# Kernel tuning notes

Hardware: AMD Instinct MI355X
Metric: run time of the kernel (lower is better)

Reference implementation:

```python
import jax, jax.numpy as jnp
import numpy as np

HIDDEN = 2048  # hidden_size; also key seq length (required by span_param broadcast)
BATCH = 4
SEQ = 2048


def setup_inputs() -> dict:
    key = jax.random.key(0)
    kq, kk, kv = jax.random.split(key, 3)
    return {
        "query": jax.random.normal(kq, (BATCH, SEQ, HIDDEN), dtype=jnp.float32),
        "key": jax.random.normal(kk, (BATCH, SEQ, HIDDEN), dtype=jnp.float32),
        "value": jax.random.normal(kv, (BATCH, SEQ, HIDDEN), dtype=jnp.float32),
        "span_param": jnp.ones((1, HIDDEN), dtype=jnp.float32),  # nn.Parameter init torch.ones
    }


def reference(query, key, value, span_param):
    # scores: [B, Sq, Sk]
    scale = 1.0 / jnp.sqrt(jnp.asarray(query.shape[-1], query.dtype))
    scores = jnp.einsum("bqd,bkd->bqk", query, key) * scale
    # elementwise learned gate broadcast over last axis (Sk == hidden_size)
    scores = scores * jax.nn.sigmoid(span_param)
    weights = jax.nn.softmax(scores, axis=-1)
    return jnp.einsum("bqk,bkd->bqd", weights, value)
```

## Files before the change

kernel.cpp:

```cpp
#include <hip/hip_runtime.h>
#include <math.h>


#define SEQ 2048
#define HID 2048
#define NB 4

typedef __attribute__((ext_vector_type(8))) __bf16 bf16x8;
typedef __attribute__((ext_vector_type(4))) float f32x4;
typedef __attribute__((ext_vector_type(8))) unsigned short ushort8;

#define GLD16(src, dst)                                              \
  __builtin_amdgcn_global_load_lds(                                  \
      (const __attribute__((address_space(1))) void*)(src),          \
      (__attribute__((address_space(3))) void*)(dst), 16, 0, 0)

__device__ __forceinline__ unsigned short f2bf(float f) {
  unsigned u = __float_as_uint(f);
  u += 0x7fffu + ((u >> 16) & 1u);
  return (unsigned short)(u >> 16);
}

__global__ __launch_bounds__(256) void cvt_kernel(
    const float* __restrict__ in, unsigned short* __restrict__ out, int n) {
  size_t stride = (size_t)gridDim.x * blockDim.x * 8;
  for (size_t i = ((size_t)blockIdx.x * blockDim.x + threadIdx.x) * 8;
       i < (size_t)n; i += stride) {
    float4 v0 = *reinterpret_cast<const float4*>(in + i);
    float4 v1 = *reinterpret_cast<const float4*>(in + i + 4);
    ushort8 o;
    o[0] = f2bf(v0.x); o[1] = f2bf(v0.y); o[2] = f2bf(v0.z); o[3] = f2bf(v0.w);
    o[4] = f2bf(v1.x); o[5] = f2bf(v1.y); o[6] = f2bf(v1.z); o[7] = f2bf(v1.w);
    *reinterpret_cast<ushort8*>(out + i) = o;
  }
}

__global__ __launch_bounds__(256) void tcvt_kernel(
    const float* __restrict__ V, unsigned short* __restrict__ Vt) {
  __shared__ unsigned short tile[64][65];
  int b = blockIdx.z;
  int k0 = blockIdx.x * 64;
  int d0 = blockIdx.y * 64;
  const float* src = V + ((size_t)b * SEQ + k0) * HID + d0;
  unsigned short* dst = Vt + ((size_t)b * HID + d0) * SEQ + k0;
  int t = threadIdx.x;
#pragma unroll
  for (int i = 0; i < 4; ++i) {
    int j = i * 256 + t;
    int r = j >> 4;
    int c = (j & 15) * 4;
    float4 v = *reinterpret_cast<const float4*>(src + (size_t)r * HID + c);
    tile[c + 0][r] = f2bf(v.x);
    tile[c + 1][r] = f2bf(v.y);
    tile[c + 2][r] = f2bf(v.z);
    tile[c + 3][r] = f2bf(v.w);
  }
  __syncthreads();
#pragma unroll
  for (int i = 0; i < 2; ++i) {
    int j = i * 256 + t;
    int r = j >> 3;
    int c = (j & 7) * 8;
    ushort8 o;
#pragma unroll
    for (int e = 0; e < 8; ++e) o[e] = tile[r][c + e];
    *reinterpret_cast<ushort8*>(dst + (size_t)r * SEQ + c) = o;
  }
}

__global__ __launch_bounds__(256) void gemm1_kernel(
    const unsigned short* __restrict__ Q, const unsigned short* __restrict__ K,
    unsigned short* __restrict__ E, float* __restrict__ Z,
    const float* __restrict__ span) {
  __shared__ __align__(16) unsigned short Asm[128 * 64];
  __shared__ __align__(16) unsigned short Bsm[128 * 64];
  int bid = blockIdx.x;
  int swz = (bid & 7) * ((int)gridDim.x >> 3) + (bid >> 3);
  int b = swz >> 8;
  int tl = swz & 255;
  int brow = tl >> 4, bcol = tl & 15;
  const unsigned short* A = Q + (size_t)b * SEQ * HID + (size_t)brow * 128 * HID;
  const unsigned short* B = K + (size_t)b * SEQ * HID + (size_t)bcol * 128 * HID;
  unsigned short* Eb = E + (size_t)b * SEQ * SEQ;
  float* Zb = Z + b * SEQ;

  int tid = threadIdx.x;
  int l = tid & 63, w = tid >> 6;
  const unsigned short* agA[4];
  const unsigned short* agB[4];
  int ldsOfs[4];
#pragma unroll
  for (int i = 0; i < 4; ++i) {
    int j = i * 256 + tid;
    int row = j >> 3, kc = (j & 7) * 8;
    agA[i] = A + (size_t)row * HID + kc;
    agB[i] = B + (size_t)row * HID + kc;
    ldsOfs[i] = (i * 256 + w * 64) * 8;
  }
  f32x4 acc[4][4];
#pragma unroll
  for (int m = 0; m < 4; ++m)
#pragma unroll
    for (int n = 0; n < 4; ++n) acc[m][n] = (f32x4){0.f, 0.f, 0.f, 0.f};

  int wr = w >> 1, wc = w & 1;
  int lr = l & 15, lh = l >> 4;

  for (int kt = 0; kt < HID / 64; ++kt) {
    if (kt) __syncthreads();
#pragma unroll
    for (int i = 0; i < 4; ++i) GLD16(agA[i] + kt * 64, Asm + ldsOfs[i]);
#pragma unroll
    for (int i = 0; i < 4; ++i) GLD16(agB[i] + kt * 64, Bsm + ldsOfs[i]);
    __syncthreads();
#pragma unroll
    for (int kk = 0; kk < 2; ++kk) {
      bf16x8 af[4], bfr[4];
#pragma unroll
      for (int m = 0; m < 4; ++m)
        af[m] = *reinterpret_cast<const bf16x8*>(
            &Asm[(wr * 64 + m * 16 + lr) * 64 + kk * 32 + lh * 8]);
#pragma unroll
      for (int n = 0; n < 4; ++n)
        bfr[n] = *reinterpret_cast<const bf16x8*>(
            &Bsm[(wc * 64 + n * 16 + lr) * 64 + kk * 32 + lh * 8]);
#pragma unroll
      for (int m = 0; m < 4; ++m)
#pragma unroll
        for (int n = 0; n < 4; ++n)
          acc[m][n] =
              __builtin_amdgcn_mfma_f32_16x16x32_bf16(af[m], bfr[n], acc[m][n], 0, 0, 0);
    }
  }

  const float scale = 0.02209708691207961f;
  float g[4];
  int coln[4];
#pragma unroll
  for (int n = 0; n < 4; ++n) {
    int col = bcol * 128 + wc * 64 + n * 16 + lr;
    coln[n] = col;
    g[n] = scale / (1.0f + __expf(-span[col]));
  }
#pragma unroll
  for (int m = 0; m < 4; ++m) {
    int rbase = brow * 128 + wr * 64 + m * 16 + lh * 4;
#pragma unroll
    for (int j = 0; j < 4; ++j) {
      int q = rbase + j;
      float rs = 0.f;
#pragma unroll
      for (int n = 0; n < 4; ++n) {
        float e = __expf(acc[m][n][j] * g[n]);
        Eb[(size_t)q * SEQ + coln[n]] = f2bf(e);
        rs += e;
      }
      rs += __shfl_xor(rs, 1, 16);
      rs += __shfl_xor(rs, 2, 16);
      rs += __shfl_xor(rs, 4, 16);
      rs += __shfl_xor(rs, 8, 16);
      if (lr == 0) atomicAdd(&Zb[q], rs);
    }
  }
}

__global__ __launch_bounds__(256) void gemm2_kernel(
    const unsigned short* __restrict__ E, const unsigned short* __restrict__ Vt,
    float* __restrict__ Out, const float* __restrict__ Z) {
  __shared__ __align__(16) unsigned short Asm[128 * 64];
  __shared__ __align__(16) unsigned short Bsm[128 * 64];
  int bid = blockIdx.x;
  int swz = (bid & 7) * ((int)gridDim.x >> 3) + (bid >> 3);
  int b = swz >> 8;
  int tl = swz & 255;
  int brow = tl >> 4, bcol = tl & 15;
  const unsigned short* A = E + (size_t)b * SEQ * SEQ + (size_t)brow * 128 * SEQ;
  const unsigned short* B = Vt + (size_t)b * HID * SEQ + (size_t)bcol * 128 * SEQ;
  float* Outb = Out + (size_t)b * SEQ * HID;
  const float* Zb = Z + b * SEQ;

  int tid = threadIdx.x;
  int l = tid & 63, w = tid >> 6;
  const unsigned short* agA[4];
  const unsigned short* agB[4];
  int ldsOfs[4];
#pragma unroll
  for (int i = 0; i < 4; ++i) {
    int j = i * 256 + tid;
    int row = j >> 3, kc = (j & 7) * 8;
    agA[i] = A + (size_t)row * SEQ + kc;
    agB[i] = B + (size_t)row * SEQ + kc;
    ldsOfs[i] = (i * 256 + w * 64) * 8;
  }
  f32x4 acc[4][4];
#pragma unroll
  for (int m = 0; m < 4; ++m)
#pragma unroll
    for (int n = 0; n < 4; ++n) acc[m][n] = (f32x4){0.f, 0.f, 0.f, 0.f};

  int wr = w >> 1, wc = w & 1;
  int lr = l & 15, lh = l >> 4;

  for (int kt = 0; kt < SEQ / 64; ++kt) {
    if (kt) __syncthreads();
#pragma unroll
    for (int i = 0; i < 4; ++i) GLD16(agA[i] + kt * 64, Asm + ldsOfs[i]);
#pragma unroll
    for (int i = 0; i < 4; ++i) GLD16(agB[i] + kt * 64, Bsm + ldsOfs[i]);
    __syncthreads();
#pragma unroll
    for (int kk = 0; kk < 2; ++kk) {
      bf16x8 af[4], bfr[4];
#pragma unroll
      for (int m = 0; m < 4; ++m)
        af[m] = *reinterpret_cast<const bf16x8*>(
            &Asm[(wr * 64 + m * 16 + lr) * 64 + kk * 32 + lh * 8]);
#pragma unroll
      for (int n = 0; n < 4; ++n)
        bfr[n] = *reinterpret_cast<const bf16x8*>(
            &Bsm[(wc * 64 + n * 16 + lr) * 64 + kk * 32 + lh * 8]);
#pragma unroll
      for (int m = 0; m < 4; ++m)
#pragma unroll
        for (int n = 0; n < 4; ++n)
          acc[m][n] =
              __builtin_amdgcn_mfma_f32_16x16x32_bf16(af[m], bfr[n], acc[m][n], 0, 0, 0);
    }
  }

#pragma unroll
  for (int m = 0; m < 4; ++m) {
    int rbase = brow * 128 + wr * 64 + m * 16 + lh * 4;
#pragma unroll
    for (int j = 0; j < 4; ++j) {
      int q = rbase + j;
      float zi = 1.0f / Zb[q];
#pragma unroll
      for (int n = 0; n < 4; ++n) {
        int col = bcol * 128 + wc * 64 + n * 16 + lr;
        Outb[(size_t)q * HID + col] = acc[m][n][j] * zi;
      }
    }
  }
}

extern "C" void kernel_launch(void* const* d_in, const int* in_sizes, int n_in,
                              void* d_out, int out_size, void* d_ws, size_t ws_size,
                              hipStream_t stream) {
  const float* Q = (const float*)d_in[0];
  const float* K = (const float*)d_in[1];
  const float* V = (const float*)d_in[2];
  const float* span = (const float*)d_in[3];
  float* out = (float*)d_out;
  char* ws = (char*)d_ws;

  const size_t TEN = (size_t)NB * SEQ * HID;
  unsigned short* Qb = (unsigned short*)(ws);
  unsigned short* Kb = (unsigned short*)(ws + TEN * 2);
  unsigned short* Vt = (unsigned short*)(ws + TEN * 4);
  unsigned short* E  = (unsigned short*)(ws + TEN * 6);
  float* Z = (float*)(ws + TEN * 8);

  hipMemsetAsync(Z, 0, (size_t)NB * SEQ * sizeof(float), stream);
  cvt_kernel<<<4096, 256, 0, stream>>>(Q, Qb, (int)TEN);
  cvt_kernel<<<4096, 256, 0, stream>>>(K, Kb, (int)TEN);
  tcvt_kernel<<<dim3(SEQ / 64, HID / 64, NB), 256, 0, stream>>>(V, Vt);
  gemm1_kernel<<<1024, 256, 0, stream>>>(Qb, Kb, E, Z, span);
  gemm2_kernel<<<1024, 256, 0, stream>>>(E, Vt, out, Z);
}
```

Before: 439.7 us.

## Rewrite GEMMs with 256x256 tiles, 4-stage LDS pipeline, swizzled LDS

Both GEMMs are replaced by one templated kernel that uses 512 threads and 256x256 output tiles. It keeps a 4-deep ring of 32-wide K slices in LDS, loaded with global_load_lds and waited on with explicit vmcnt and barriers. LDS reads use an XOR swizzle to avoid bank conflicts, and MFMA sections run at raised priority. The Q and K conversions are merged into one launch. Larger tiles cut global traffic per FLOP and the pipeline hides load latency, but the grid shrinks to 256 blocks, there are more registers per thread, and the hand-written waitcnt logic is fragile.

```diff
diff --git a/kernel.cpp b/kernel.cpp
--- a/kernel.cpp
+++ b/kernel.cpp
@@ -5,6 +5,7 @@
 #define SEQ 2048
 #define HID 2048
 #define NB 4
+#define S 2048
 
 typedef __attribute__((ext_vector_type(8))) __bf16 bf16x8;
 typedef __attribute__((ext_vector_type(4))) float f32x4;
@@ -21,11 +22,17 @@
   return (unsigned short)(u >> 16);
 }
 
-__global__ __launch_bounds__(256) void cvt_kernel(
-    const float* __restrict__ in, unsigned short* __restrict__ out, int n) {
-  size_t stride = (size_t)gridDim.x * blockDim.x * 8;
-  for (size_t i = ((size_t)blockIdx.x * blockDim.x + threadIdx.x) * 8;
-       i < (size_t)n; i += stride) {
+__global__ __launch_bounds__(256) void cvt2_kernel(
+    const float* __restrict__ q, const float* __restrict__ k,
+    unsigned short* __restrict__ qb, unsigned short* __restrict__ kb) {
+  const size_t n = (size_t)NB * SEQ * HID;
+  int half = gridDim.x >> 1;
+  const float* in;
+  unsigned short* out;
+  int bx = blockIdx.x;
+  if (bx < half) { in = q; out = qb; } else { in = k; out = kb; bx -= half; }
+  size_t stride = (size_t)half * blockDim.x * 8;
+  for (size_t i = ((size_t)bx * blockDim.x + threadIdx.x) * 8; i < n; i += stride) {
     float4 v0 = *reinterpret_cast<const float4*>(in + i);
     float4 v1 = *reinterpret_cast<const float4*>(in + i + 4);
     ushort8 o;
@@ -68,177 +75,158 @@
   }
 }
 
-__global__ __launch_bounds__(256) void gemm1_kernel(
-    const unsigned short* __restrict__ Q, const unsigned short* __restrict__ K,
-    unsigned short* __restrict__ E, float* __restrict__ Z,
-    const float* __restrict__ span) {
-  __shared__ __align__(16) unsigned short Asm[128 * 64];
-  __shared__ __align__(16) unsigned short Bsm[128 * 64];
+
+#define K_ITER(VMC, DOSTAGE)                                                  \
+  {                                                                           \
+    asm volatile("s_waitcnt vmcnt(" #VMC ")" ::: "memory");                   \
+    __builtin_amdgcn_s_barrier();                                             \
+    asm volatile("" ::: "memory");                                            \
+    int lb = (t & 3) * 16384;                                                 \
+    bf16x8 af[8], bfr[4];                                                     \
+    _Pragma("unroll")                                                         \
+    for (int m = 0; m < 4; ++m)                                               \
+      af[m] = *(const bf16x8*)&lds[lb + aOff[m]];                             \
+    _Pragma("unroll")                                                         \
+    for (int n = 0; n < 4; ++n)                                               \
+      bfr[n] = *(const bf16x8*)&lds[lb + bOff[n]];                            \
+    if (DOSTAGE) {                                                            \
+      int sb = ((t + 3) & 3) * 16384;                                         \
+      GLD16(aS0 + (size_t)(t + 3) * 32, &lds[sb + ldsA0]);                    \
+      GLD16(aS1 + (size_t)(t + 3) * 32, &lds[sb + ldsA1]);                    \
+    }                                                                         \
+    __builtin_amdgcn_s_barrier();                                             \
+    asm volatile("s_waitcnt lgkmcnt(0)" ::: "memory");                        \
+    __builtin_amdgcn_s_setprio(1);                                            \
+    _Pragma("unroll")                                                         \
+    for (int m = 0; m < 4; ++m)                                               \
+      _Pragma("unroll")                                                       \
+      for (int n = 0; n < 4; ++n)                                             \
+        acc[m][n] = __builtin_amdgcn_mfma_f32_16x16x32_bf16(af[m], bfr[n],    \
+                                                            acc[m][n], 0, 0, 0); \
+    __builtin_amdgcn_s_setprio(0);                                            \
+    __builtin_amdgcn_s_barrier();                                             \
+    asm volatile("" ::: "memory");                                            \
+    _Pragma("unroll")                                                         \
+    for (int m = 4; m < 8; ++m)                                               \
+      af[m] = *(const bf16x8*)&lds[lb + aOff[m]];                             \
+    if (DOSTAGE) {                                                            \
+      int sb = ((t + 3) & 3) * 16384;                                         \
+      GLD16(bS0 + (size_t)(t + 3) * 32, &lds[sb + ldsB0]);                    \
+      GLD16(bS1 + (size_t)(t + 3) * 32, &lds[sb + ldsB1]);                    \
+    }                                                                         \
+    asm volatile("s_waitcnt lgkmcnt(0)" ::: "memory");                        \
+    __builtin_amdgcn_s_setprio(1);                                            \
+    _Pragma("unroll")                                                         \
+    for (int m = 4; m < 8; ++m)                                               \
+      _Pragma("unroll")                                                       \
+      for (int n = 0; n < 4; ++n)                                             \
+        acc[m][n] = __builtin_amdgcn_mfma_f32_16x16x32_bf16(af[m], bfr[n],    \
+                                                            acc[m][n], 0, 0, 0); \
+    __builtin_amdgcn_s_setprio(0);                                            \
+  }
+
+template <bool IS_G1>
+__global__ __launch_bounds__(512, 2) void gemm_kernel(
+    const unsigned short* __restrict__ Amat, const unsigned short* __restrict__ Bmat,
+    void* __restrict__ outp, float* __restrict__ Z, const float* __restrict__ span) {
+  __shared__ __align__(16) unsigned short lds[4 * 16384];
+
   int bid = blockIdx.x;
-  int swz = (bid & 7) * ((int)gridDim.x >> 3) + (bid >> 3);
-  int b = swz >> 8;
-  int tl = swz & 255;
-  int brow = tl >> 4, bcol = tl & 15;
-  const unsigned short* A = Q + (size_t)b * SEQ * HID + (size_t)brow * 128 * HID;
-  const unsigned short* B = K + (size_t)b * SEQ * HID + (size_t)bcol * 128 * HID;
-  unsigned short* Eb = E + (size_t)b * SEQ * SEQ;
-  float* Zb = Z + b * SEQ;
+  int swz = (bid & 7) * 32 + (bid >> 3);
+  int b = swz >> 6;
+  int tile = swz & 63;
+  int brow = tile >> 3, bcol = tile & 7;
+  const unsigned short* A = Amat + (size_t)b * S * S + (size_t)brow * 256 * S;
+  const unsigned short* B = Bmat + (size_t)b * S * S + (size_t)bcol * 256 * S;
 
   int tid = threadIdx.x;
-  int l = tid & 63, w = tid >> 6;
-  const unsigned short* agA[4];
-  const unsigned short* agB[4];
-  int ldsOfs[4];
-#pragma unroll
-  for (int i = 0; i < 4; ++i) {
-    int j = i * 256 + tid;
-    int row = j >> 3, kc = (j & 7) * 8;
-    agA[i] = A + (size_t)row * HID + kc;
-    agB[i] = B + (size_t)row * HID + kc;
-    ldsOfs[i] = (i * 256 + w * 64) * 8;
-  }
-  f32x4 acc[4][4];
-#pragma unroll
-  for (int m = 0; m < 4; ++m)
+  int w = tid >> 6, l = tid & 63;
+  int wr = w >> 2, wc = w & 3;
+  int lr = l & 15, lh = l >> 4;
+
+  int srcSwz = ((l & 3) ^ ((l >> 3) & 3)) * 8;
+  const unsigned short* aS0 = A + (size_t)(w * 16 + (l >> 2)) * S + srcSwz;
+  const unsigned short* aS1 = aS0 + (size_t)128 * S;
+  const unsigned short* bS0 = B + (size_t)(w * 16 + (l >> 2)) * S + srcSwz;
+  const unsigned short* bS1 = bS0 + (size_t)128 * S;
+  int ldsA0 = w * 512;
+  int ldsA1 = w * 512 + 4096;
+  int ldsB0 = 8192 + w * 512;
+  int ldsB1 = 8192 + w * 512 + 4096;
+
+  int rdswz = (lh ^ ((lr >> 1) & 3)) * 8;
+  int aOff[8], bOff[4];
+#pragma unroll
+  for (int m = 0; m < 8; ++m) aOff[m] = (wr * 128 + m * 16 + lr) * 32 + rdswz;
+#pragma unroll
+  for (int n = 0; n < 4; ++n) bOff[n] = 8192 + (wc * 64 + n * 16 + lr) * 32 + rdswz;
+
+  f32x4 acc[8][4];
+#pragma unroll
+  for (int m = 0; m < 8; ++m)
 #pragma unroll
     for (int n = 0; n < 4; ++n) acc[m][n] = (f32x4){0.f, 0.f, 0.f, 0.f};
 
-  int wr = w >> 1, wc = w & 1;
-  int lr = l & 15, lh = l >> 4;
-
-  for (int kt = 0; kt < HID / 64; ++kt) {
-    if (kt) __syncthreads();
-#pragma unroll
-    for (int i = 0; i < 4; ++i) GLD16(agA[i] + kt * 64, Asm + ldsOfs[i]);
-#pragma unroll
-    for (int i = 0; i < 4; ++i) GLD16(agB[i] + kt * 64, Bsm + ldsOfs[i]);
-    __syncthreads();
-#pragma unroll
-    for (int kk = 0; kk < 2; ++kk) {
-      bf16x8 af[4], bfr[4];
-#pragma unroll
-      for (int m = 0; m < 4; ++m)
-        af[m] = *reinterpret_cast<const bf16x8*>(
-            &Asm[(wr * 64 + m * 16 + lr) * 64 + kk * 32 + lh * 8]);
-#pragma unroll
-      for (int n = 0; n < 4; ++n)
-        bfr[n] = *reinterpret_cast<const bf16x8*>(
-            &Bsm[(wc * 64 + n * 16 + lr) * 64 + kk * 32 + lh * 8]);
-#pragma unroll
-      for (int m = 0; m < 4; ++m)
-#pragma unroll
-        for (int n = 0; n < 4; ++n)
-          acc[m][n] =
-              __builtin_amdgcn_mfma_f32_16x16x32_bf16(af[m], bfr[n], acc[m][n], 0, 0, 0);
+  GLD16(aS0, &lds[ldsA0]);           GLD16(aS1, &lds[ldsA1]);
+  GLD16(bS0, &lds[ldsB0]);           GLD16(bS1, &lds[ldsB1]);
+  GLD16(aS0 + 32, &lds[16384 + ldsA0]); GLD16(aS1 + 32, &lds[16384 + ldsA1]);
+  GLD16(bS0 + 32, &lds[16384 + ldsB0]); GLD16(bS1 + 32, &lds[16384 + ldsB1]);
+  GLD16(aS0 + 64, &lds[32768 + ldsA0]); GLD16(aS1 + 64, &lds[32768 + ldsA1]);
+  GLD16(bS0 + 64, &lds[32768 + ldsB0]); GLD16(bS1 + 64, &lds[32768 + ldsB1]);
+
+  int t;
+  for (t = 0; t < 61; ++t) K_ITER(8, true);
+  K_ITER(8, false); ++t;
+  K_ITER(4, false); ++t;
+  K_ITER(0, false);
+
+  if constexpr (IS_G1) {
+    const float scale = 0.02209708691207961f;
+    float g[4];
+    int coln[4];
+#pragma unroll
+    for (int n = 0; n < 4; ++n) {
+      int col = bcol * 256 + wc * 64 + n * 16 + lr;
+      coln[n] = col;
+      g[n] = scale / (1.0f + __expf(-span[col]));
     }
-  }
-
-  const float scale = 0.02209708691207961f;
-  float g[4];
-  int coln[4];
-#pragma unroll
-  for (int n = 0; n < 4; ++n) {
-    int col = bcol * 128 + wc * 64 + n * 16 + lr;
-    coln[n] = col;
-    g[n] = scale / (1.0f + __expf(-span[col]));
-  }
-#pragma unroll
-  for (int m = 0; m < 4; ++m) {
-    int rbase = brow * 128 + wr * 64 + m * 16 + lh * 4;
-#pragma unroll
-    for (int j = 0; j < 4; ++j) {
-      int q = rbase + j;
-      float rs = 0.f;
-#pragma unroll
-      for (int n = 0; n < 4; ++n) {
-        float e = __expf(acc[m][n][j] * g[n]);
-        Eb[(size_t)q * SEQ + coln[n]] = f2bf(e);
-        rs += e;
+    unsigned short* Eb = (unsigned short*)outp + (size_t)b * S * S;
+    float* Zb = Z + b * S;
+#pragma unroll
+    for (int m = 0; m < 8; ++m) {
+      int rbase = brow * 256 + wr * 128 + m * 16 + lh * 4;
+#pragma unroll
+      for (int j = 0; j < 4; ++j) {
+        int q = rbase + j;
+        float rs = 0.f;
+#pragma unroll
+        for (int n = 0; n < 4; ++n) {
+          float e = __expf(acc[m][n][j] * g[n]);
+          Eb[(size_t)q * S + coln[n]] = f2bf(e);
+          rs += e;
+        }
+        rs += __shfl_xor(rs, 1, 16);
+        rs += __shfl_xor(rs, 2, 16);
+        rs += __shfl_xor(rs, 4, 16);
+        rs += __shfl_xor(rs, 8, 16);
+        if (lr == 0) atomicAdd(&Zb[q], rs);
       }
-      rs += __shfl_xor(rs, 1, 16);
-      rs += __shfl_xor(rs, 2, 16);
-      rs += __shfl_xor(rs, 4, 16);
-      rs += __shfl_xor(rs, 8, 16);
-      if (lr == 0) atomicAdd(&Zb[q], rs);
     }
-  }
-}
-
-__global__ __launch_bounds__(256) void gemm2_kernel(
-    const unsigned short* __restrict__ E, const unsigned short* __restrict__ Vt,
-    float* __restrict__ Out, const float* __restrict__ Z) {
-  __shared__ __align__(16) unsigned short Asm[128 * 64];
-  __shared__ __align__(16) unsigned short Bsm[128 * 64];
-  int bid = blockIdx.x;
-  int swz = (bid & 7) * ((int)gridDim.x >> 3) + (bid >> 3);
-  int b = swz >> 8;
-  int tl = swz & 255;
-  int brow = tl >> 4, bcol = tl & 15;
-  const unsigned short* A = E + (size_t)b * SEQ * SEQ + (size_t)brow * 128 * SEQ;
-  const unsigned short* B = Vt + (size_t)b * HID * SEQ + (size_t)bcol * 128 * SEQ;
-  float* Outb = Out + (size_t)b * SEQ * HID;
-  const float* Zb = Z + b * SEQ;
-
-  int tid = threadIdx.x;
-  int l = tid & 63, w = tid >> 6;
-  const unsigned short* agA[4];
-  const unsigned short* agB[4];
-  int ldsOfs[4];
-#pragma unroll
-  for (int i = 0; i < 4; ++i) {
-    int j = i * 256 + tid;
-    int row = j >> 3, kc = (j & 7) * 8;
-    agA[i] = A + (size_t)row * SEQ + kc;
-    agB[i] = B + (size_t)row * SEQ + kc;
-    ldsOfs[i] = (i * 256 + w * 64) * 8;
-  }
-  f32x4 acc[4][4];
-#pragma unroll
-  for (int m = 0; m < 4; ++m)
-#pragma unroll
-    for (int n = 0; n < 4; ++n) acc[m][n] = (f32x4){0.f, 0.f, 0.f, 0.f};
-
-  int wr = w >> 1, wc = w & 1;
-  int lr = l & 15, lh = l >> 4;
-
-  for (int kt = 0; kt < SEQ / 64; ++kt) {
-    if (kt) __syncthreads();
-#pragma unroll
-    for (int i = 0; i < 4; ++i) GLD16(agA[i] + kt * 64, Asm + ldsOfs[i]);
-#pragma unroll
-    for (int i = 0; i < 4; ++i) GLD16(agB[i] + kt * 64, Bsm + ldsOfs[i]);
-    __syncthreads();
-#pragma unroll
-    for (int kk = 0; kk < 2; ++kk) {
-      bf16x8 af[4], bfr[4];
-#pragma unroll
-      for (int m = 0; m < 4; ++m)
-        af[m] = *reinterpret_cast<const bf16x8*>(
-            &Asm[(wr * 64 + m * 16 + lr) * 64 + kk * 32 + lh * 8]);
-#pragma unroll
-      for (int n = 0; n < 4; ++n)
-        bfr[n] = *reinterpret_cast<const bf16x8*>(
-            &Bsm[(wc * 64 + n * 16 + lr) * 64 + kk * 32 + lh * 8]);
-#pragma unroll
-      for (int m = 0; m < 4; ++m)
-#pragma unroll
-        for (int n = 0; n < 4; ++n)
-          acc[m][n] =
-              __builtin_amdgcn_mfma_f32_16x16x32_bf16(af[m], bfr[n], acc[m][n], 0, 0, 0);
-    }
-  }
-
-#pragma unroll
-  for (int m = 0; m < 4; ++m) {
-    int rbase = brow * 128 + wr * 64 + m * 16 + lh * 4;
-#pragma unroll
-    for (int j = 0; j < 4; ++j) {
-      int q = rbase + j;
-      float zi = 1.0f / Zb[q];
-#pragma unroll
-      for (int n = 0; n < 4; ++n) {
-        int col = bcol * 128 + wc * 64 + n * 16 + lr;
-        Outb[(size_t)q * HID + col] = acc[m][n][j] * zi;
+  } else {
+    float* Ob = (float*)outp + (size_t)b * S * S;
+    const float* Zb = Z + b * S;
+#pragma unroll
+    for (int m = 0; m < 8; ++m) {
+      int rbase = brow * 256 + wr * 128 + m * 16 + lh * 4;
+#pragma unroll
+      for (int j = 0; j < 4; ++j) {
+        int q = rbase + j;
+        float zi = 1.0f / Zb[q];
+#pragma unroll
+        for (int n = 0; n < 4; ++n) {
+          int col = bcol * 256 + wc * 64 + n * 16 + lr;
+          Ob[(size_t)q * S + col] = acc[m][n][j] * zi;
+        }
       }
     }
   }
@@ -251,7 +239,6 @@
   const float* K = (const float*)d_in[1];
   const float* V = (const float*)d_in[2];
   const float* span = (const float*)d_in[3];
-  float* out = (float*)d_out;
   char* ws = (char*)d_ws;
 
   const size_t TEN = (size_t)NB * SEQ * HID;
@@ -262,9 +249,8 @@
   float* Z = (float*)(ws + TEN * 8);
 
   hipMemsetAsync(Z, 0, (size_t)NB * SEQ * sizeof(float), stream);
-  cvt_kernel<<<4096, 256, 0, stream>>>(Q, Qb, (int)TEN);
-  cvt_kernel<<<4096, 256, 0, stream>>>(K, Kb, (int)TEN);
+  cvt2_kernel<<<8192, 256, 0, stream>>>(Q, K, Qb, Kb);
   tcvt_kernel<<<dim3(SEQ / 64, HID / 64, NB), 256, 0, stream>>>(V, Vt);
-  gemm1_kernel<<<1024, 256, 0, stream>>>(Qb, Kb, E, Z, span);
-  gemm2_kernel<<<1024, 256, 0, stream>>>(E, Vt, out, Z);
-}
+  gemm_kernel<true><<<256, 512, 0, stream>>>(Qb, Kb, E, Z, span);
+  gemm_kernel<false><<<256, 512, 0, stream>>>(E, Vt, d_out, Z, nullptr);
+}
```

After: 355.1 us. 1.24x faster.
